# Kernel tuning notes

Measured on AMD Instinct MI355X. Metric: run time of the kernel, lower is better.

## Reference

```python
import jax, jax.numpy as jnp
import numpy as np

N = 50000
E = 800000
NUM_KINDS = 100
D_NODE = 64
D_EDGE = 4
D_MSG = 64
L = 3
D_IN = 2 * D_NODE + D_EDGE  # 132


def setup_inputs() -> dict:
    key = jax.random.key(0)
    ks = jax.random.split(key, 20)

    def w(k, shape, fan_in):
        bound = 1.0 / np.sqrt(fan_in)
        return jax.random.uniform(k, shape, jnp.float32, -bound, bound)

    inp = {
        "edge_index": jax.random.randint(ks[0], (2, E), 0, N),
        "node_kind_ids": jax.random.randint(ks[1], (N,), 0, NUM_KINDS),
        "edge_attr": jax.random.normal(ks[2], (E, D_EDGE), jnp.float32),
        # learned params
        "emb": jax.random.normal(ks[3], (NUM_KINDS, D_NODE), jnp.float32),
        # stacked per-layer message MLP params [L, ...]
        "msg_w1": w(ks[4], (L, D_MSG, D_IN), D_IN),
        "msg_b1": w(ks[5], (L, D_MSG), D_IN),
        "msg_w2": w(ks[6], (L, D_MSG, D_MSG), D_MSG),
        "msg_b2": w(ks[7], (L, D_MSG), D_MSG),
        # stacked per-layer GRUCell params (torch layout: [3*d_node, d_in])
        "gru_wih": w(ks[8], (L, 3 * D_NODE, D_MSG), D_NODE),
        "gru_whh": w(ks[9], (L, 3 * D_NODE, D_NODE), D_NODE),
        "gru_bih": w(ks[10], (L, 3 * D_NODE), D_NODE),
        "gru_bhh": w(ks[11], (L, 3 * D_NODE), D_NODE),
        # edge head: Linear(132,64) -> SiLU -> Linear(64,1)
        "head_w1": w(ks[12], (64, D_IN), D_IN),
        "head_b1": w(ks[13], (64,), D_IN),
        "head_w2": w(ks[14], (1, 64), 64),
        "head_b2": w(ks[15], (1,), 64),
    }
    return inp


def reference(edge_index, node_kind_ids, edge_attr, emb,
              msg_w1, msg_b1, msg_w2, msg_b2,
              gru_wih, gru_whh, gru_bih, gru_bhh,
              head_w1, head_b1, head_w2, head_b2):
    src, dst = edge_index[0], edge_index[1]
    h = emb[node_kind_ids]  # [N, d_node]
    n_nodes = h.shape[0]
    for l in range(L):
        x = jnp.concatenate([h[src], h[dst], edge_attr], axis=1)  # [E, 132]
        m = jax.nn.silu(x @ msg_w1[l].T + msg_b1[l]) @ msg_w2[l].T + msg_b2[l]  # [E, d_msg]
        agg = jax.ops.segment_sum(m, dst, num_segments=n_nodes)  # [N, d_msg]
        # torch GRUCell math
        gi = agg @ gru_wih[l].T + gru_bih[l]  # [N, 3*d_node]
        gh = h @ gru_whh[l].T + gru_bhh[l]
        ir, iz, inn = jnp.split(gi, 3, axis=1)
        hr, hz, hn = jnp.split(gh, 3, axis=1)
        r = jax.nn.sigmoid(ir + hr)
        z = jax.nn.sigmoid(iz + hz)
        n = jnp.tanh(inn + r * hn)
        h = (1.0 - z) * n + z * h
    x = jnp.concatenate([h[src], h[dst], edge_attr], axis=1)  # [E, 132]
    logits = (jax.nn.silu(x @ head_w1.T + head_b1) @ head_w2.T + head_b2)[:, 0]
    return jax.nn.sigmoid(logits)  # [E]
```

## Files before the change

kernel.cpp:

```cpp
#include <hip/hip_runtime.h>
#include <hip/hip_bf16.h>


typedef __attribute__((ext_vector_type(8))) short bf16x8;
typedef __attribute__((ext_vector_type(4))) float f32x4;
#define MFMA16(a, b, c) __builtin_amdgcn_mfma_f32_16x16x32_bf16(a, b, c, 0, 0, 0)

#define CHUNK 128
#define XSTRIDE 336
#define MSTRIDE 264
#define HSTRIDE 144
#define SLABSZ 10752
#define HIDSZ  4608

#define WRZST 264
#define WNST  136

__device__ __forceinline__ float fast_sig(float x) { return 1.f / (1.f + __expf(-x)); }
__device__ __forceinline__ float fast_tanh(float x) {
    float ax = fabsf(x);
    float t = __expf(-2.f * ax);
    return copysignf((1.f - t) / (1.f + t), x);
}
__device__ __forceinline__ ushort f2bf(float f) {
    unsigned u = __float_as_uint(f);
    unsigned r = u + 0x7FFF + ((u >> 16) & 1);
    return (ushort)(r >> 16);
}

__global__ void prep_kernel(const float* __restrict__ msg_w1,
                            const float* __restrict__ msg_w2,
                            const float* __restrict__ gru_wih,
                            const float* __restrict__ gru_whh,
                            const float* __restrict__ head_w1,
                            const float* __restrict__ head_w2,
                            ushort* __restrict__ Wb1, ushort* __restrict__ Wb2,
                            ushort* __restrict__ Wh1, ushort* __restrict__ Wh2b,
                            ushort* __restrict__ Wrz, ushort* __restrict__ Wni,
                            ushort* __restrict__ Wnh) {
    int t = blockIdx.x * 256 + threadIdx.x;
    if (t < 30720) {
        int l = t / 10240, r = t % 10240, j = r / 160, k = r % 160;
        Wb1[t] = (k < 132) ? f2bf(msg_w1[l * 8448 + j * 132 + k]) : 0;
        return;
    }
    t -= 30720;
    if (t < 12288) {
        Wb2[t] = f2bf(msg_w2[t]);
        return;
    }
    t -= 12288;
    if (t < 10240) {
        int j = t / 160, k = t % 160;
        Wh1[t] = (k < 132) ? f2bf(head_w1[j * 132 + k]) : 0;
        return;
    }
    t -= 10240;
    if (t < 1024) {
        int j = t >> 6, k = t & 63;
        Wh2b[t] = (j == 0) ? f2bf(head_w2[k]) : 0;
        return;
    }
    t -= 1024;
    if (t < 49152) {
        int l = t / 16384, r = t % 16384, n = r >> 7, k = r & 127;
        float v = (k < 64) ? gru_wih[l * 12288 + n * 64 + k]
                           : gru_whh[l * 12288 + n * 64 + (k - 64)];
        Wrz[t] = f2bf(v);
        return;
    }
    t -= 49152;
    if (t < 12288) {
        int l = t / 4096, r = t % 4096, j = r >> 6, k = r & 63;
        Wni[t] = f2bf(gru_wih[l * 12288 + (128 + j) * 64 + k]);
        return;
    }
    t -= 12288;
    if (t < 12288) {
        int l = t / 4096, r = t % 4096, j = r >> 6, k = r & 63;
        Wnh[t] = f2bf(gru_whh[l * 12288 + (128 + j) * 64 + k]);
    }
}

__global__ void embed_kernel(float* __restrict__ h, ushort* __restrict__ hb,
                             const float* __restrict__ emb,
                             const int* __restrict__ kinds, int N) {
    int t = blockIdx.x * 256 + threadIdx.x;
    if (t >= N * 64) return;
    int node = t >> 6, d = t & 63;
    float v = emb[kinds[node] * 64 + d];
    h[t] = v;
    hb[t] = f2bf(v);
}

__global__ void hist_kernel(const int* __restrict__ dst, int* __restrict__ deg, int E) {
    int e = blockIdx.x * 256 + threadIdx.x;
    if (e < E) atomicAdd(&deg[dst[e]], 1);
}

__global__ void scan_kernel(const int* __restrict__ deg, int* __restrict__ cursor, int N) {
    __shared__ int sums[1024];
    int tid = threadIdx.x;
    int chunk = (N + 1023) >> 10;
    int lo = tid * chunk, hi = min(lo + chunk, N);
    int s = 0;
    for (int i = lo; i < hi; i++) s += deg[i];
    sums[tid] = s;
    __syncthreads();
    for (int off = 1; off < 1024; off <<= 1) {
        int v = (tid >= off) ? sums[tid - off] : 0;
        __syncthreads();
        sums[tid] += v;
        __syncthreads();
    }
    int run = (tid > 0) ? sums[tid - 1] : 0;
    for (int i = lo; i < hi; i++) {
        cursor[i] = run;
        run += deg[i];
    }
}

__global__ void scatter_kernel(const int* __restrict__ src, const int* __restrict__ dst,
                               const float* __restrict__ ea, int* __restrict__ cursor,
                               int* __restrict__ src_s, int* __restrict__ dst_s,
                               ushort* __restrict__ ea_sb, int E) {
    int e = blockIdx.x * 256 + threadIdx.x;
    if (e >= E) return;
    int d = dst[e];
    int p = atomicAdd(&cursor[d], 1);
    src_s[p] = src[e];
    dst_s[p] = d;
    float4 e4 = ((const float4*)ea)[e];
    ushort4 eb;
    eb.x = f2bf(e4.x); eb.y = f2bf(e4.y); eb.z = f2bf(e4.z); eb.w = f2bf(e4.w);
    ((ushort4*)ea_sb)[p] = eb;
}

__global__ __launch_bounds__(256) void edge_msg_mfma(
    const ushort* __restrict__ hb, const int* __restrict__ src_s,
    const int* __restrict__ dst_s, const ushort* __restrict__ ea_sb,
    const ushort* __restrict__ Wb1l, const ushort* __restrict__ Wb2l,
    const float* __restrict__ b1, const float* __restrict__ b2,
    float* __restrict__ agg, int E, int nchunks) {
    __shared__ char lds[4 * SLABSZ + 4 * HIDSZ];
    int tid = threadIdx.x;
    int w = tid >> 6, lane = tid & 63;
    int quad = lane >> 4, nrow = lane & 15;
    char* slab = lds + w * SLABSZ;
    char* hidb = lds + 4 * SLABSZ + w * HIDSZ;

    bf16x8 wf1[4][5], wf2[4][2];
    float b1v[4], b2v[4];
#pragma unroll
    for (int nt = 0; nt < 4; nt++) {
        int n = nt * 16 + nrow;
#pragma unroll
        for (int ks = 0; ks < 5; ks++)
            wf1[nt][ks] = *(const bf16x8*)(Wb1l + n * 160 + ks * 32 + quad * 8);
#pragma unroll
        for (int ks = 0; ks < 2; ks++)
            wf2[nt][ks] = *(const bf16x8*)(Wb2l + n * 64 + ks * 32 + quad * 8);
        b1v[nt] = b1[n];
        b2v[nt] = b2[n];
    }

    for (int chunk = blockIdx.x; chunk < nchunks; chunk += gridDim.x) {
        int ebase = chunk * CHUNK;
        {
            int el = tid >> 1, half = tid & 1;
            int r = el & 31;
            int ec = min(ebase + el, E - 1);
            int node = half ? dst_s[ec] : src_s[ec];
            const float4* hrow = (const float4*)(hb + (size_t)node * 64);
            float4* xw = (float4*)(slab + r * XSTRIDE + half * 128);
#pragma unroll
            for (int i = 0; i < 8; i++) xw[i] = hrow[i];
            if (half == 0) {
                *(uint2*)(slab + r * XSTRIDE + 256) = *(const uint2*)(ea_sb + (size_t)ec * 4);
            } else {
                uint2 z2 = {0u, 0u};
                float4 z4 = {0.f, 0.f, 0.f, 0.f};
                *(uint2*)(slab + r * XSTRIDE + 264) = z2;
                *(float4*)(slab + r * XSTRIDE + 272) = z4;
                *(float4*)(slab + r * XSTRIDE + 288) = z4;
                *(float4*)(slab + r * XSTRIDE + 304) = z4;
            }
        }
        f32x4 acc1[2][4];
#pragma unroll
        for (int mt = 0; mt < 2; mt++)
#pragma unroll
            for (int nt = 0; nt < 4; nt++) {
                f32x4 v;
                v[0] = v[1] = v[2] = v[3] = b1v[nt];
                acc1[mt][nt] = v;
            }
#pragma unroll
        for (int ks = 0; ks < 5; ks++) {
            bf16x8 a0 = *(const bf16x8*)(slab + nrow * XSTRIDE + ks * 64 + quad * 16);
            bf16x8 a1 = *(const bf16x8*)(slab + (16 + nrow) * XSTRIDE + ks * 64 + quad * 16);
#pragma unroll
            for (int nt = 0; nt < 4; nt++) {
                acc1[0][nt] = MFMA16(a0, wf1[nt][ks], acc1[0][nt]);
                acc1[1][nt] = MFMA16(a1, wf1[nt][ks], acc1[1][nt]);
            }
        }
#pragma unroll
        for (int mt = 0; mt < 2; mt++)
#pragma unroll
            for (int nt = 0; nt < 4; nt++)
#pragma unroll
                for (int rg = 0; rg < 4; rg++) {
                    float v = acc1[mt][nt][rg];
                    v = v * fast_sig(v);
                    int rm = mt * 16 + quad * 4 + rg;
                    *(ushort*)(hidb + rm * HSTRIDE + (nt * 16 + nrow) * 2) = f2bf(v);
                }
        f32x4 acc2[2][4];
#pragma unroll
        for (int mt = 0; mt < 2; mt++)
#pragma unroll
            for (int nt = 0; nt < 4; nt++) {
                f32x4 v;
                v[0] = v[1] = v[2] = v[3] = b2v[nt];
                acc2[mt][nt] = v;
            }
#pragma unroll
        for (int ks = 0; ks < 2; ks++) {
            bf16x8 a0 = *(const bf16x8*)(hidb + nrow * HSTRIDE + ks * 64 + quad * 16);
            bf16x8 a1 = *(const bf16x8*)(hidb + (16 + nrow) * HSTRIDE + ks * 64 + quad * 16);
#pragma unroll
            for (int nt = 0; nt < 4; nt++) {
                acc2[0][nt] = MFMA16(a0, wf2[nt][ks], acc2[0][nt]);
                acc2[1][nt] = MFMA16(a1, wf2[nt][ks], acc2[1][nt]);
            }
        }
#pragma unroll
        for (int mt = 0; mt < 2; mt++)
#pragma unroll
            for (int nt = 0; nt < 4; nt++)
#pragma unroll
                for (int rg = 0; rg < 4; rg++) {
                    int rm = mt * 16 + quad * 4 + rg;
                    *(float*)(slab + rm * MSTRIDE + (nt * 16 + nrow) * 4) = acc2[mt][nt][rg];
                }
        {
            int e32 = ebase + w * 32;
            int dmy = dst_s[min(e32 + (lane & 31), E - 1)];
            int limit = min(32, E - e32);
            int nx = __shfl_down(dmy, 1);
            bool tl = ((lane & 31) == 31) || (dmy != nx);
            unsigned long long tm = __ballot(tl);
            float run = 0.f;
#pragma unroll
            for (int i = 0; i < 32; i++) {
                if (i < limit) {
                    run += *(const float*)(slab + i * MSTRIDE + lane * 4);
                    if (((tm >> i) & 1ull) || (i + 1 == limit)) {
                        int di = __shfl(dmy, i);
                        unsafeAtomicAdd(&agg[(size_t)di * 64 + lane], run);
                        run = 0.f;
                    }
                }
            }
        }
    }
}

__global__ __launch_bounds__(256) void head_mfma(
    const ushort* __restrict__ hb, const int* __restrict__ src,
    const int* __restrict__ dst, const float* __restrict__ ea,
    const ushort* __restrict__ Wh1, const ushort* __restrict__ Wh2b,
    const float* __restrict__ hb1, const float* __restrict__ hb2p,
    float* __restrict__ out, int E, int nchunks) {
    __shared__ char lds[4 * SLABSZ + 4 * HIDSZ];
    int tid = threadIdx.x;
    int w = tid >> 6, lane = tid & 63;
    int quad = lane >> 4, nrow = lane & 15;
    char* slab = lds + w * SLABSZ;
    char* hidb = lds + 4 * SLABSZ + w * HIDSZ;

    bf16x8 wf1[4][5], wh2[2];
    float b1v[4];
#pragma unroll
    for (int nt = 0; nt < 4; nt++) {
        int n = nt * 16 + nrow;
#pragma unroll
        for (int ks = 0; ks < 5; ks++)
            wf1[nt][ks] = *(const bf16x8*)(Wh1 + n * 160 + ks * 32 + quad * 8);
        b1v[nt] = hb1[n];
    }
#pragma unroll
    for (int ks = 0; ks < 2; ks++)
        wh2[ks] = *(const bf16x8*)(Wh2b + nrow * 64 + ks * 32 + quad * 8);
    float hb2 = hb2p[0];

    for (int chunk = blockIdx.x; chunk < nchunks; chunk += gridDim.x) {
        int ebase = chunk * CHUNK;
        {
            int el = tid >> 1, half = tid & 1;
            int r = el & 31;
            int ec = min(ebase + el, E - 1);
            int node = half ? dst[ec] : src[ec];
            const float4* hrow = (const float4*)(hb + (size_t)node * 64);
            float4* xw = (float4*)(slab + r * XSTRIDE + half * 128);
#pragma unroll
            for (int i = 0; i < 8; i++) xw[i] = hrow[i];
            if (half == 0) {
                float4 e4 = ((const float4*)ea)[ec];
                ushort4 eb;
                eb.x = f2bf(e4.x); eb.y = f2bf(e4.y); eb.z = f2bf(e4.z); eb.w = f2bf(e4.w);
                *(ushort4*)(slab + r * XSTRIDE + 256) = eb;
            } else {
                uint2 z2 = {0u, 0u};
                float4 z4 = {0.f, 0.f, 0.f, 0.f};
                *(uint2*)(slab + r * XSTRIDE + 264) = z2;
                *(float4*)(slab + r * XSTRIDE + 272) = z4;
                *(float4*)(slab + r * XSTRIDE + 288) = z4;
                *(float4*)(slab + r * XSTRIDE + 304) = z4;
            }
        }
        f32x4 acc1[2][4];
#pragma unroll
        for (int mt = 0; mt < 2; mt++)
#pragma unroll
            for (int nt = 0; nt < 4; nt++) {
                f32x4 v;
                v[0] = v[1] = v[2] = v[3] = b1v[nt];
                acc1[mt][nt] = v;
            }
#pragma unroll
        for (int ks = 0; ks < 5; ks++) {
            bf16x8 a0 = *(const bf16x8*)(slab + nrow * XSTRIDE + ks * 64 + quad * 16);
            bf16x8 a1 = *(const bf16x8*)(slab + (16 + nrow) * XSTRIDE + ks * 64 + quad * 16);
#pragma unroll
            for (int nt = 0; nt < 4; nt++) {
                acc1[0][nt] = MFMA16(a0, wf1[nt][ks], acc1[0][nt]);
                acc1[1][nt] = MFMA16(a1, wf1[nt][ks], acc1[1][nt]);
            }
        }
#pragma unroll
        for (int mt = 0; mt < 2; mt++)
#pragma unroll
            for (int nt = 0; nt < 4; nt++)
#pragma unroll
                for (int rg = 0; rg < 4; rg++) {
                    float v = acc1[mt][nt][rg];
                    v = v * fast_sig(v);
                    int rm = mt * 16 + quad * 4 + rg;
                    *(ushort*)(hidb + rm * HSTRIDE + (nt * 16 + nrow) * 2) = f2bf(v);
                }
        f32x4 acc3[2];
#pragma unroll
        for (int mt = 0; mt < 2; mt++) {
            f32x4 v;
            v[0] = v[1] = v[2] = v[3] = 0.f;
            acc3[mt] = v;
        }
#pragma unroll
        for (int ks = 0; ks < 2; ks++) {
            bf16x8 a0 = *(const bf16x8*)(hidb + nrow * HSTRIDE + ks * 64 + quad * 16);
            bf16x8 a1 = *(const bf16x8*)(hidb + (16 + nrow) * HSTRIDE + ks * 64 + quad * 16);
            acc3[0] = MFMA16(a0, wh2[ks], acc3[0]);
            acc3[1] = MFMA16(a1, wh2[ks], acc3[1]);
        }
        if (nrow == 0) {
#pragma unroll
            for (int mt = 0; mt < 2; mt++)
#pragma unroll
                for (int rg = 0; rg < 4; rg++) {
                    int e = ebase + w * 32 + mt * 16 + quad * 4 + rg;
                    if (e < E) out[e] = fast_sig(acc3[mt][rg] + hb2);
                }
        }
    }
}

__device__ __forceinline__ bf16x8 aggfrag(const float* __restrict__ row, int off) {
    float4 f0 = *(const float4*)(row + off);
    float4 f1 = *(const float4*)(row + off + 4);
    bf16x8 r;
    r[0] = (short)f2bf(f0.x); r[1] = (short)f2bf(f0.y);
    r[2] = (short)f2bf(f0.z); r[3] = (short)f2bf(f0.w);
    r[4] = (short)f2bf(f1.x); r[5] = (short)f2bf(f1.y);
    r[6] = (short)f2bf(f1.z); r[7] = (short)f2bf(f1.w);
    return r;
}

__global__ __launch_bounds__(256) void gru_mfma(
    float* __restrict__ h, ushort* __restrict__ hb, const float* __restrict__ agg,
    const ushort* __restrict__ Wrzg, const ushort* __restrict__ Wnig,
    const ushort* __restrict__ Wnhg,
    const float* __restrict__ bih, const float* __restrict__ bhh, int N) {
    __shared__ char lds[128 * WRZST + 2 * 64 * WNST];
    int tid = threadIdx.x, w = tid >> 6, lane = tid & 63;
    int quad = lane >> 4, nrow = lane & 15;
    char* wrz = lds;
    char* wni = lds + 128 * WRZST;
    char* wnh = wni + 64 * WNST;

    {
        int r = tid >> 1, half = tid & 1;
        const uint4* g = (const uint4*)(Wrzg + r * 128 + half * 64);
        uint4* d = (uint4*)(wrz + r * WRZST + half * 128);
#pragma unroll
        for (int i = 0; i < 8; i++) d[i] = g[i];
        if (tid < 128) {
            const uint4* g2 = (const uint4*)(Wnig + (tid >> 1) * 64 + (tid & 1) * 32);
            uint4* d2 = (uint4*)(wni + (tid >> 1) * WNST + (tid & 1) * 64);
#pragma unroll
            for (int i = 0; i < 4; i++) d2[i] = g2[i];
        } else {
            int t2 = tid - 128;
            const uint4* g2 = (const uint4*)(Wnhg + (t2 >> 1) * 64 + (t2 & 1) * 32);
            uint4* d2 = (uint4*)(wnh + (t2 >> 1) * WNST + (t2 & 1) * 64);
#pragma unroll
            for (int i = 0; i < 4; i++) d2[i] = g2[i];
        }
    }
    __syncthreads();

    int nb0 = blockIdx.x * 128 + w * 32;
    if (nb0 >= N) return;

    float brz[8], bi[4], bhv[4];
#pragma unroll
    for (int nt = 0; nt < 8; nt++) brz[nt] = bih[nt * 16 + nrow] + bhh[nt * 16 + nrow];
#pragma unroll
    for (int nt = 0; nt < 4; nt++) {
        bi[nt] = bih[128 + nt * 16 + nrow];
        bhv[nt] = bhh[128 + nt * 16 + nrow];
    }

    int n0 = min(nb0 + nrow, N - 1);
    int n1 = min(nb0 + 16 + nrow, N - 1);
    const float* ag0 = agg + (size_t)n0 * 64;
    const float* ag1 = agg + (size_t)n1 * 64;
    const ushort* hb0 = hb + (size_t)n0 * 64;
    const ushort* hb1 = hb + (size_t)n1 * 64;

    f32x4 accrz[2][8], acci[2][4], acch[2][4];
#pragma unroll
    for (int nt = 0; nt < 8; nt++) {
        f32x4 v; v[0] = v[1] = v[2] = v[3] = brz[nt];
        accrz[0][nt] = v; accrz[1][nt] = v;
    }
#pragma unroll
    for (int nt = 0; nt < 4; nt++) {
        f32x4 vi; vi[0] = vi[1] = vi[2] = vi[3] = bi[nt];
        acci[0][nt] = vi; acci[1][nt] = vi;
        f32x4 vh; vh[0] = vh[1] = vh[2] = vh[3] = bhv[nt];
        acch[0][nt] = vh; acch[1][nt] = vh;
    }

#pragma unroll
    for (int ks = 0; ks < 4; ks++) {
        bf16x8 a0, a1;
        if (ks < 2) {
            a0 = aggfrag(ag0, ks * 32 + quad * 8);
            a1 = aggfrag(ag1, ks * 32 + quad * 8);
        } else {
            a0 = *(const bf16x8*)(hb0 + (ks - 2) * 32 + quad * 8);
            a1 = *(const bf16x8*)(hb1 + (ks - 2) * 32 + quad * 8);
        }
#pragma unroll
        for (int nt = 0; nt < 8; nt++) {
            bf16x8 b = *(const bf16x8*)(wrz + (nt * 16 + nrow) * WRZST + ks * 64 + quad * 16);
            accrz[0][nt] = MFMA16(a0, b, accrz[0][nt]);
            accrz[1][nt] = MFMA16(a1, b, accrz[1][nt]);
        }
        if (ks < 2) {
#pragma unroll
            for (int nt = 0; nt < 4; nt++) {
                bf16x8 b = *(const bf16x8*)(wni + (nt * 16 + nrow) * WNST + ks * 64 + quad * 16);
                acci[0][nt] = MFMA16(a0, b, acci[0][nt]);
                acci[1][nt] = MFMA16(a1, b, acci[1][nt]);
            }
        } else {
#pragma unroll
            for (int nt = 0; nt < 4; nt++) {
                bf16x8 b = *(const bf16x8*)(wnh + (nt * 16 + nrow) * WNST + (ks - 2) * 64 + quad * 16);
                acch[0][nt] = MFMA16(a0, b, acch[0][nt]);
                acch[1][nt] = MFMA16(a1, b, acch[1][nt]);
            }
        }
    }

#pragma unroll
    for (int mt = 0; mt < 2; mt++)
#pragma unroll
        for (int nt = 0; nt < 4; nt++)
#pragma unroll
            for (int rg = 0; rg < 4; rg++) {
                int node = nb0 + mt * 16 + quad * 4 + rg;
                if (node < N) {
                    int col = nt * 16 + nrow;
                    float r = fast_sig(accrz[mt][nt][rg]);
                    float z = fast_sig(accrz[mt][nt + 4][rg]);
                    float nn = fast_tanh(acci[mt][nt][rg] + r * acch[mt][nt][rg]);
                    size_t idx = (size_t)node * 64 + col;
                    float ho = h[idx];
                    float hnew = (1.f - z) * nn + z * ho;
                    h[idx] = hnew;
                    hb[idx] = f2bf(hnew);
                }
            }
}

extern "C" void kernel_launch(void* const* d_in, const int* in_sizes, int n_in,
                              void* d_out, int out_size, void* d_ws, size_t ws_size,
                              hipStream_t stream) {
    const int* edge_index = (const int*)d_in[0];
    int E = in_sizes[0] / 2;
    const int* src = edge_index;
    const int* dst = edge_index + E;
    const int* kinds = (const int*)d_in[1];
    int N = in_sizes[1];
    const float* edge_attr = (const float*)d_in[2];
    const float* emb = (const float*)d_in[3];
    const float* msg_w1 = (const float*)d_in[4];
    const float* msg_b1 = (const float*)d_in[5];
    const float* msg_w2 = (const float*)d_in[6];
    const float* msg_b2 = (const float*)d_in[7];
    const float* gru_wih = (const float*)d_in[8];
    const float* gru_whh = (const float*)d_in[9];
    const float* gru_bih = (const float*)d_in[10];
    const float* gru_bhh = (const float*)d_in[11];
    const float* head_w1 = (const float*)d_in[12];
    const float* head_b1 = (const float*)d_in[13];
    const float* head_w2 = (const float*)d_in[14];
    const float* head_b2 = (const float*)d_in[15];
    float* out = (float*)d_out;

    char* p = (char*)d_ws;
    float* h = (float*)p;        p += (size_t)N * 64 * 4;
    float* agg = (float*)p;      p += (size_t)N * 64 * 4;
    int* deg = (int*)p;          p += (size_t)N * 4;
    int* cursor = (int*)p;       p += (size_t)N * 4;
    int* src_s = (int*)p;        p += (size_t)E * 4;
    int* dst_s = (int*)p;        p += (size_t)E * 4;
    ushort* hb = (ushort*)p;     p += (size_t)N * 64 * 2;
    ushort* Wb1 = (ushort*)p;    p += 30720 * 2;
    ushort* Wb2 = (ushort*)p;    p += 12288 * 2;
    ushort* Wh1 = (ushort*)p;    p += 10240 * 2;
    ushort* Wh2b = (ushort*)p;   p += 1024 * 2;
    ushort* Wrz = (ushort*)p;    p += 49152 * 2;
    ushort* Wni = (ushort*)p;    p += 12288 * 2;
    ushort* Wnh = (ushort*)p;    p += 12288 * 2;
    ushort* ea_sb = (ushort*)p;  p += (size_t)E * 4 * 2;

    int nchunks = (E + CHUNK - 1) / CHUNK;

    prep_kernel<<<500, 256, 0, stream>>>(msg_w1, msg_w2, gru_wih, gru_whh, head_w1,
                                         head_w2, Wb1, Wb2, Wh1, Wh2b, Wrz, Wni, Wnh);
    embed_kernel<<<(N * 64 + 255) / 256, 256, 0, stream>>>(h, hb, emb, kinds, N);

    hipMemsetAsync(deg, 0, (size_t)N * sizeof(int), stream);
    hist_kernel<<<(E + 255) / 256, 256, 0, stream>>>(dst, deg, E);
    scan_kernel<<<1, 1024, 0, stream>>>(deg, cursor, N);
    scatter_kernel<<<(E + 255) / 256, 256, 0, stream>>>(src, dst, edge_attr, cursor,
                                                        src_s, dst_s, ea_sb, E);

    for (int l = 0; l < 3; l++) {
        hipMemsetAsync(agg, 0, (size_t)N * 64 * sizeof(float), stream);
        edge_msg_mfma<<<512, 256, 0, stream>>>(
            hb, src_s, dst_s, ea_sb,
            Wb1 + l * 10240, Wb2 + l * 4096,
            msg_b1 + l * 64, msg_b2 + l * 64, agg, E, nchunks);
        gru_mfma<<<(N + 127) / 128, 256, 0, stream>>>(
            h, hb, agg, Wrz + l * 16384, Wni + l * 4096, Wnh + l * 4096,
            gru_bih + l * 192, gru_bhh + l * 192, N);
    }
    head_mfma<<<512, 256, 0, stream>>>(hb, src, dst, edge_attr, Wh1, Wh2b,
                                       head_b1, head_b2, out, E, nchunks);
}
```

Measured before the change: 685.9 us.

## Feed edge attributes via registers, shrink LDS slab, fuse agg zeroing into GRU

The edge-attribute K-slice of the first MLP GEMM now comes straight from registers as an MFMA A-fragment. Before, it was staged and zero-padded in LDS. This lets the per-wave slab stride shrink, cutting LDS per block so more blocks can be resident; launch bounds are raised to 3 blocks per CU and the grid to 2048. The per-layer memset of the aggregation buffer is replaced by zeroing agg rows at the end of the GRU kernel, with one memset up front. The risks are higher register pressure from the extra weight fragments and correctness that depends on each GRU wave owning its rows.

```diff
diff --git a/kernel.cpp b/kernel.cpp
--- a/kernel.cpp
+++ b/kernel.cpp
@@ -7,10 +7,10 @@
 #define MFMA16(a, b, c) __builtin_amdgcn_mfma_f32_16x16x32_bf16(a, b, c, 0, 0, 0)
 
 #define CHUNK 128
-#define XSTRIDE 336
+#define XSTRIDE 272
 #define MSTRIDE 264
 #define HSTRIDE 144
-#define SLABSZ 10752
+#define SLABSZ 8704
 #define HIDSZ  4608
 
 #define WRZST 264
@@ -136,7 +136,7 @@
     ((ushort4*)ea_sb)[p] = eb;
 }
 
-__global__ __launch_bounds__(256) void edge_msg_mfma(
+__global__ __launch_bounds__(256, 3) void edge_msg_mfma(
     const ushort* __restrict__ hb, const int* __restrict__ src_s,
     const int* __restrict__ dst_s, const ushort* __restrict__ ea_sb,
     const ushort* __restrict__ Wb1l, const ushort* __restrict__ Wb2l,
@@ -149,14 +149,15 @@
     char* slab = lds + w * SLABSZ;
     char* hidb = lds + 4 * SLABSZ + w * HIDSZ;
 
-    bf16x8 wf1[4][5], wf2[4][2];
+    bf16x8 wf1[4][4], wfea[4], wf2[4][2];
     float b1v[4], b2v[4];
 #pragma unroll
     for (int nt = 0; nt < 4; nt++) {
         int n = nt * 16 + nrow;
 #pragma unroll
-        for (int ks = 0; ks < 5; ks++)
+        for (int ks = 0; ks < 4; ks++)
             wf1[nt][ks] = *(const bf16x8*)(Wb1l + n * 160 + ks * 32 + quad * 8);
+        wfea[nt] = *(const bf16x8*)(Wb1l + n * 160 + 128 + quad * 8);
 #pragma unroll
         for (int ks = 0; ks < 2; ks++)
             wf2[nt][ks] = *(const bf16x8*)(Wb2l + n * 64 + ks * 32 + quad * 8);
@@ -175,16 +176,14 @@
             float4* xw = (float4*)(slab + r * XSTRIDE + half * 128);
 #pragma unroll
             for (int i = 0; i < 8; i++) xw[i] = hrow[i];
-            if (half == 0) {
-                *(uint2*)(slab + r * XSTRIDE + 256) = *(const uint2*)(ea_sb + (size_t)ec * 4);
-            } else {
-                uint2 z2 = {0u, 0u};
-                float4 z4 = {0.f, 0.f, 0.f, 0.f};
-                *(uint2*)(slab + r * XSTRIDE + 264) = z2;
-                *(float4*)(slab + r * XSTRIDE + 272) = z4;
-                *(float4*)(slab + r * XSTRIDE + 288) = z4;
-                *(float4*)(slab + r * XSTRIDE + 304) = z4;
-            }
+        }
+        bf16x8 ea0 = {0, 0, 0, 0, 0, 0, 0, 0};
+        bf16x8 ea1 = {0, 0, 0, 0, 0, 0, 0, 0};
+        if (quad == 0) {
+            int ec0 = min(ebase + w * 32 + nrow, E - 1);
+            int ec1 = min(ebase + w * 32 + 16 + nrow, E - 1);
+            *(uint2*)&ea0 = *(const uint2*)(ea_sb + (size_t)ec0 * 4);
+            *(uint2*)&ea1 = *(const uint2*)(ea_sb + (size_t)ec1 * 4);
         }
         f32x4 acc1[2][4];
 #pragma unroll
@@ -196,7 +195,7 @@
                 acc1[mt][nt] = v;
             }
 #pragma unroll
-        for (int ks = 0; ks < 5; ks++) {
+        for (int ks = 0; ks < 4; ks++) {
             bf16x8 a0 = *(const bf16x8*)(slab + nrow * XSTRIDE + ks * 64 + quad * 16);
             bf16x8 a1 = *(const bf16x8*)(slab + (16 + nrow) * XSTRIDE + ks * 64 + quad * 16);
 #pragma unroll
@@ -204,6 +203,11 @@
                 acc1[0][nt] = MFMA16(a0, wf1[nt][ks], acc1[0][nt]);
                 acc1[1][nt] = MFMA16(a1, wf1[nt][ks], acc1[1][nt]);
             }
+        }
+#pragma unroll
+        for (int nt = 0; nt < 4; nt++) {
+            acc1[0][nt] = MFMA16(ea0, wfea[nt], acc1[0][nt]);
+            acc1[1][nt] = MFMA16(ea1, wfea[nt], acc1[1][nt]);
         }
 #pragma unroll
         for (int mt = 0; mt < 2; mt++)
@@ -267,7 +271,7 @@
     }
 }
 
-__global__ __launch_bounds__(256) void head_mfma(
+__global__ __launch_bounds__(256, 3) void head_mfma(
     const ushort* __restrict__ hb, const int* __restrict__ src,
     const int* __restrict__ dst, const float* __restrict__ ea,
     const ushort* __restrict__ Wh1, const ushort* __restrict__ Wh2b,
@@ -280,14 +284,15 @@
     char* slab = lds + w * SLABSZ;
     char* hidb = lds + 4 * SLABSZ + w * HIDSZ;
 
-    bf16x8 wf1[4][5], wh2[2];
+    bf16x8 wf1[4][4], wfea[4], wh2[2];
     float b1v[4];
 #pragma unroll
     for (int nt = 0; nt < 4; nt++) {
         int n = nt * 16 + nrow;
 #pragma unroll
-        for (int ks = 0; ks < 5; ks++)
+        for (int ks = 0; ks < 4; ks++)
             wf1[nt][ks] = *(const bf16x8*)(Wh1 + n * 160 + ks * 32 + quad * 8);
+        wfea[nt] = *(const bf16x8*)(Wh1 + n * 160 + 128 + quad * 8);
         b1v[nt] = hb1[n];
     }
 #pragma unroll
@@ -306,19 +311,19 @@
             float4* xw = (float4*)(slab + r * XSTRIDE + half * 128);
 #pragma unroll
             for (int i = 0; i < 8; i++) xw[i] = hrow[i];
-            if (half == 0) {
-                float4 e4 = ((const float4*)ea)[ec];
-                ushort4 eb;
-                eb.x = f2bf(e4.x); eb.y = f2bf(e4.y); eb.z = f2bf(e4.z); eb.w = f2bf(e4.w);
-                *(ushort4*)(slab + r * XSTRIDE + 256) = eb;
-            } else {
-                uint2 z2 = {0u, 0u};
-                float4 z4 = {0.f, 0.f, 0.f, 0.f};
-                *(uint2*)(slab + r * XSTRIDE + 264) = z2;
-                *(float4*)(slab + r * XSTRIDE + 272) = z4;
-                *(float4*)(slab + r * XSTRIDE + 288) = z4;
-                *(float4*)(slab + r * XSTRIDE + 304) = z4;
-            }
+        }
+        bf16x8 ea0 = {0, 0, 0, 0, 0, 0, 0, 0};
+        bf16x8 ea1 = {0, 0, 0, 0, 0, 0, 0, 0};
+        if (quad == 0) {
+            int ec0 = min(ebase + w * 32 + nrow, E - 1);
+            int ec1 = min(ebase + w * 32 + 16 + nrow, E - 1);
+            float4 e0 = ((const float4*)ea)[ec0];
+            float4 e1 = ((const float4*)ea)[ec1];
+            ushort4 u0, u1;
+            u0.x = f2bf(e0.x); u0.y = f2bf(e0.y); u0.z = f2bf(e0.z); u0.w = f2bf(e0.w);
+            u1.x = f2bf(e1.x); u1.y = f2bf(e1.y); u1.z = f2bf(e1.z); u1.w = f2bf(e1.w);
+            *(ushort4*)&ea0 = u0;
+            *(ushort4*)&ea1 = u1;
         }
         f32x4 acc1[2][4];
 #pragma unroll
@@ -330,7 +335,7 @@
                 acc1[mt][nt] = v;
             }
 #pragma unroll
-        for (int ks = 0; ks < 5; ks++) {
+        for (int ks = 0; ks < 4; ks++) {
             bf16x8 a0 = *(const bf16x8*)(slab + nrow * XSTRIDE + ks * 64 + quad * 16);
             bf16x8 a1 = *(const bf16x8*)(slab + (16 + nrow) * XSTRIDE + ks * 64 + quad * 16);
 #pragma unroll
@@ -338,6 +343,11 @@
                 acc1[0][nt] = MFMA16(a0, wf1[nt][ks], acc1[0][nt]);
                 acc1[1][nt] = MFMA16(a1, wf1[nt][ks], acc1[1][nt]);
             }
+        }
+#pragma unroll
+        for (int nt = 0; nt < 4; nt++) {
+            acc1[0][nt] = MFMA16(ea0, wfea[nt], acc1[0][nt]);
+            acc1[1][nt] = MFMA16(ea1, wfea[nt], acc1[1][nt]);
         }
 #pragma unroll
         for (int mt = 0; mt < 2; mt++)
@@ -388,7 +398,7 @@
 }
 
 __global__ __launch_bounds__(256) void gru_mfma(
-    float* __restrict__ h, ushort* __restrict__ hb, const float* __restrict__ agg,
+    float* __restrict__ h, ushort* __restrict__ hb, float* __restrict__ agg,
     const ushort* __restrict__ Wrzg, const ushort* __restrict__ Wnig,
     const ushort* __restrict__ Wnhg,
     const float* __restrict__ bih, const float* __restrict__ bhh, int N) {
@@ -505,6 +515,24 @@
                     hb[idx] = f2bf(hnew);
                 }
             }
+
+    {
+        float4 z4 = {0.f, 0.f, 0.f, 0.f};
+        if (nb0 + nrow < N) {
+            float* a = agg + (size_t)(nb0 + nrow) * 64;
+            *(float4*)(a + quad * 8) = z4;
+            *(float4*)(a + quad * 8 + 4) = z4;
+            *(float4*)(a + 32 + quad * 8) = z4;
+            *(float4*)(a + 32 + quad * 8 + 4) = z4;
+        }
+        if (nb0 + 16 + nrow < N) {
+            float* a = agg + (size_t)(nb0 + 16 + nrow) * 64;
+            *(float4*)(a + quad * 8) = z4;
+            *(float4*)(a + quad * 8 + 4) = z4;
+            *(float4*)(a + 32 + quad * 8) = z4;
+            *(float4*)(a + 32 + quad * 8 + 4) = z4;
+        }
+    }
 }
 
 extern "C" void kernel_launch(void* const* d_in, const int* in_sizes, int n_in,
@@ -556,14 +584,14 @@
     embed_kernel<<<(N * 64 + 255) / 256, 256, 0, stream>>>(h, hb, emb, kinds, N);
 
     hipMemsetAsync(deg, 0, (size_t)N * sizeof(int), stream);
+    hipMemsetAsync(agg, 0, (size_t)N * 64 * sizeof(float), stream);
     hist_kernel<<<(E + 255) / 256, 256, 0, stream>>>(dst, deg, E);
     scan_kernel<<<1, 1024, 0, stream>>>(deg, cursor, N);
     scatter_kernel<<<(E + 255) / 256, 256, 0, stream>>>(src, dst, edge_attr, cursor,
                                                         src_s, dst_s, ea_sb, E);
 
     for (int l = 0; l < 3; l++) {
-        hipMemsetAsync(agg, 0, (size_t)N * 64 * sizeof(float), stream);
-        edge_msg_mfma<<<512, 256, 0, stream>>>(
+        edge_msg_mfma<<<2048, 256, 0, stream>>>(
             hb, src_s, dst_s, ea_sb,
             Wb1 + l * 10240, Wb2 + l * 4096,
             msg_b1 + l * 64, msg_b2 + l * 64, agg, E, nchunks);
@@ -571,6 +599,6 @@
             h, hb, agg, Wrz + l * 16384, Wni + l * 4096, Wnh + l * 4096,
             gru_bih + l * 192, gru_bhh + l * 192, N);
     }
-    head_mfma<<<512, 256, 0, stream>>>(hb, src, dst, edge_attr, Wh1, Wh2b,
-                                       head_b1, head_b2, out, E, nchunks);
-}
+    head_mfma<<<2048, 256, 0, stream>>>(hb, src, dst, edge_attr, Wh1, Wh2b,
+                                        head_b1, head_b2, out, E, nchunks);
+}
```

Result: slower. 839.8 us (+22.5%).
